# Optimization experiments

Measured on AMD Instinct MI355X. Metric: run time of the kernel, lower is better.

Reference implementation:

```python
import jax, jax.numpy as jnp
import numpy as np

EPS = 1e-8  # torch.cosine_similarity eps


def setup_inputs() -> dict:
    key = jax.random.key(0)
    k1, k2 = jax.random.split(key)
    N, D, TOPIC_E, NT = 4096, 512, 10, 6  # NT = topic_e - topic_s + 1
    x = jax.random.normal(k1, (N, D), dtype=jnp.float32)
    # H mimics the concatenated, abs()'d H_list: (input_feature, topic_e, num_topics)
    H = jax.random.uniform(k2, (D, TOPIC_E, NT), dtype=jnp.float32)
    return {"x": x, "H": H}


def reference(x, H):
    N, D = x.shape
    num_topics = H.shape[2]

    # W_list[n, t, i] = (x @ H[:, :, i])[n, t]
    W_list = jnp.einsum('nd,dti->nti', x, H)          # (N, topic_e, num_topics)
    W_max = jnp.argmax(W_list, axis=1)                # (N, num_topics), int

    # cosine similarity matrix S[a, b] = cos(x[a], x[b]) (symmetric)
    norms = jnp.maximum(jnp.linalg.norm(x, axis=1), EPS)  # (N,)
    xn = x / norms[:, None]
    S = xn @ xn.T                                      # (N, N)

    # topic-match fraction F[a, b] = mean_k [W_max[a,k] == W_max[b,k]] (symmetric)
    comp = (W_max[:, None, :] == W_max[None, :, :])    # (N, N, num_topics) bool
    F = comp.sum(axis=2).astype(jnp.float32) / num_topics

    # C[a, b] = topic_count * sim; new_nodes[b] = mean_a C[a,b] * cat(x[b], x[a])
    C = F * S                                          # (N, N)
    col_mean = C.mean(axis=0)                          # (N,) mean over a
    out_first = x * col_mean[:, None]                  # (N, D): x[b] * mean_a C[a,b]
    out_second = (C.T @ x) / N                         # (N, D): (1/N) sum_a C[a,b] x[a]
    return jnp.concatenate([out_first, out_second], axis=1)  # (N, 2D)
```

## Files before the change

### kernel.cpp

```cpp
#include <hip/hip_runtime.h>
#include <hip/hip_bf16.h>

#define DD 512
#define NTOP 10
#define NTK 6
#define NPAIR 60

typedef float f32x4 __attribute__((ext_vector_type(4)));
typedef short bf16x8 __attribute__((ext_vector_type(8)));
typedef unsigned short us8 __attribute__((ext_vector_type(8)));
typedef unsigned short us4 __attribute__((ext_vector_type(4)));

__device__ __forceinline__ void gload16(const void* g, void* l) {
  __builtin_amdgcn_global_load_lds(
      (const __attribute__((address_space(1))) unsigned int*)g,
      (__attribute__((address_space(3))) unsigned int*)l, 16, 0, 0);
}

__global__ __launch_bounds__(256) void kern_wmax(
    const float* __restrict__ x, const float* __restrict__ H,
    int* __restrict__ codes, float* __restrict__ inv_norm,
    float* __restrict__ col_sum)
{
  __shared__ float xs[4][DD];
  __shared__ float w[4][NPAIR];
  const int wv = threadIdx.x >> 6, lane = threadIdx.x & 63;
  const int n = blockIdx.x * 4 + wv;
  const float* xr = x + (size_t)n * DD;
  float ss = 0.f;
#pragma unroll
  for (int j = 0; j < 2; ++j) {
    float4 v = *(const float4*)(xr + j * 256 + lane * 4);
    *(float4*)&xs[wv][j * 256 + lane * 4] = v;
    ss = fmaf(v.x, v.x, fmaf(v.y, v.y, fmaf(v.z, v.z, fmaf(v.w, v.w, ss))));
  }
#pragma unroll
  for (int off = 32; off; off >>= 1) ss += __shfl_xor(ss, off);
  if (lane == 0) inv_norm[n] = 1.0f / fmaxf(sqrtf(ss), 1e-8f);
  __syncthreads();
  if (lane < NPAIR) {
    float acc = 0.f;
#pragma unroll 8
    for (int d = 0; d < DD; ++d) acc = fmaf(xs[wv][d], H[d * NPAIR + lane], acc);
    w[wv][lane] = acc;
  }
  __syncthreads();
  int myc = 0;
  if (lane < NTK) {
    float best = w[wv][lane];
    int bi = 0;
#pragma unroll
    for (int t = 1; t < NTOP; ++t) {
      float v = w[wv][t * NTK + lane];
      if (v > best) { best = v; bi = t; }
    }
    myc = bi << (4 * lane);
  }
#pragma unroll
  for (int off = 1; off <= 4; off <<= 1) myc |= __shfl_xor(myc, off);
  if (lane == 0) { codes[n] = myc; col_sum[n] = 0.f; }
}

__global__ __launch_bounds__(256) void kern_prep(
    const float* __restrict__ x, const float* __restrict__ inv_norm,
    __hip_bfloat16* __restrict__ xn, __hip_bfloat16* __restrict__ xT, int N)
{
  __shared__ float tile[64][65];
  const int n0 = blockIdx.x * 64, d0 = blockIdx.y * 64;
  const int tid = threadIdx.x;
  const int r = tid >> 2, cseg = (tid & 3) * 16;
  const float* src = x + (size_t)(n0 + r) * DD + d0 + cseg;
  const float invn = inv_norm[n0 + r];
  unsigned short hb[16];
#pragma unroll
  for (int q = 0; q < 4; ++q) {
    float4 v = *(const float4*)(src + q * 4);
    tile[r][cseg + q * 4 + 0] = v.x; tile[r][cseg + q * 4 + 1] = v.y;
    tile[r][cseg + q * 4 + 2] = v.z; tile[r][cseg + q * 4 + 3] = v.w;
    hb[q * 4 + 0] = __builtin_bit_cast(unsigned short, __float2bfloat16(v.x * invn));
    hb[q * 4 + 1] = __builtin_bit_cast(unsigned short, __float2bfloat16(v.y * invn));
    hb[q * 4 + 2] = __builtin_bit_cast(unsigned short, __float2bfloat16(v.z * invn));
    hb[q * 4 + 3] = __builtin_bit_cast(unsigned short, __float2bfloat16(v.w * invn));
  }
  us8 v0, v1;
#pragma unroll
  for (int i = 0; i < 8; ++i) { v0[i] = hb[i]; v1[i] = hb[i + 8]; }
  *(us8*)(xn + (size_t)(n0 + r) * DD + d0 + cseg) = v0;
  *(us8*)(xn + (size_t)(n0 + r) * DD + d0 + cseg + 8) = v1;
  __syncthreads();
  const int drow = tid >> 2, nseg = (tid & 3) * 16;
  unsigned short hb2[16];
#pragma unroll
  for (int i = 0; i < 16; ++i)
    hb2[i] = __builtin_bit_cast(unsigned short, __float2bfloat16(tile[nseg + i][drow]));
  us8 w0, w1;
#pragma unroll
  for (int i = 0; i < 8; ++i) { w0[i] = hb2[i]; w1[i] = hb2[i + 8]; }
  *(us8*)(xT + (size_t)(d0 + drow) * N + n0 + nseg) = w0;
  *(us8*)(xT + (size_t)(d0 + drow) * N + n0 + nseg + 8) = w1;
}

#define GBM 128
#define GBK 64

__global__ __launch_bounds__(512, 4) void kern_gram(
    const __hip_bfloat16* __restrict__ xn, const int* __restrict__ codes,
    __hip_bfloat16* __restrict__ Cb, float* __restrict__ col_sum, int N)
{
  __shared__ __hip_bfloat16 lds[2 * GBM * GBK];
  __shared__ float csA[GBM], csB[GBM];
  __hip_bfloat16* As = lds;
  __hip_bfloat16* Bs = lds + GBM * GBK;
  const int tid = threadIdx.x;

  int idx = blockIdx.x, ai = 0, rem = N / GBM;
  while (idx >= rem) { idx -= rem; ++ai; --rem; }
  const int bi = ai + idx;
  const bool diag = (ai == bi);
  const int a0 = ai * GBM, b0 = bi * GBM;

  if (tid < GBM) { csA[tid] = 0.f; csB[tid] = 0.f; }

  const int lane = tid & 63, wid = tid >> 6;
  const int wr = wid >> 2, wc = wid & 3;

  const f32x4 fz = {0.f, 0.f, 0.f, 0.f};
  f32x4 acc[4][2];
#pragma unroll
  for (int m = 0; m < 4; ++m)
#pragma unroll
    for (int n = 0; n < 2; ++n) acc[m][n] = fz;

  int ldsoff[2]; size_t srcA[2], srcB[2];
#pragma unroll
  for (int i = 0; i < 2; ++i) {
    int p = i * 8192 + tid * 16;
    int row = p >> 7, c = (p >> 4) & 7;
    ldsoff[i] = p;
    size_t cc = (size_t)((c ^ (row & 7)) << 4);
    srcA[i] = (size_t)(a0 + row) * (DD * 2) + cc;
    srcB[i] = (size_t)(b0 + row) * (DD * 2) + cc;
  }
  const char* xc = (const char*)xn;

  for (int kc = 0; kc < DD * 2; kc += GBK * 2) {
#pragma unroll
    for (int i = 0; i < 2; ++i) {
      gload16(xc + srcA[i] + kc, (char*)As + ldsoff[i]);
      gload16(xc + srcB[i] + kc, (char*)Bs + ldsoff[i]);
    }
    __syncthreads();
#pragma unroll
    for (int kk = 0; kk < 2; ++kk) {
      const int kb = kk * 64 + (lane >> 4) * 16;
      bf16x8 af[4], bfr[2];
#pragma unroll
      for (int m = 0; m < 4; ++m) {
        int r = wr * 64 + m * 16 + (lane & 15);
        af[m] = *(const bf16x8*)((const char*)As + r * 128 + (kb ^ ((r & 7) << 4)));
      }
#pragma unroll
      for (int n = 0; n < 2; ++n) {
        int r = wc * 32 + n * 16 + (lane & 15);
        bfr[n] = *(const bf16x8*)((const char*)Bs + r * 128 + (kb ^ ((r & 7) << 4)));
      }
#pragma unroll
      for (int m = 0; m < 4; ++m)
#pragma unroll
        for (int n = 0; n < 2; ++n)
          acc[m][n] = __builtin_amdgcn_mfma_f32_16x16x32_bf16(af[m], bfr[n], acc[m][n], 0, 0, 0);
    }
    __syncthreads();
  }

  char* ldsb = (char*)lds;
  const int rq = (lane >> 4) << 2;
  int cb[2];
#pragma unroll
  for (int n = 0; n < 2; ++n) cb[n] = codes[b0 + wc * 32 + n * 16 + (lane & 15)];

  us4 tvs[4][2];
  float colpart[2] = {0.f, 0.f};
  float rowpart[4][4] = {};
#pragma unroll
  for (int m = 0; m < 4; ++m) {
    int ca[4];
#pragma unroll
    for (int j = 0; j < 4; ++j) ca[j] = codes[a0 + wr * 64 + m * 16 + rq + j];
#pragma unroll
    for (int n = 0; n < 2; ++n) {
      const int col = wc * 32 + n * 16 + (lane & 15);
#pragma unroll
      for (int j = 0; j < 4; ++j) {
        int t = ca[j] ^ cb[n];
        t |= t >> 1; t |= t >> 2;
        t &= 0x111111;
        float f = (float)(6 - __popc(t)) * (1.0f / 6.0f);
        float cv = acc[m][n][j] * f;
        colpart[n] += cv;
        rowpart[m][j] += cv;
        __hip_bfloat16 hv = __float2bfloat16(cv);
        tvs[m][n][j] = __builtin_bit_cast(unsigned short, hv);
        const int row = wr * 64 + m * 16 + rq + j;
        const int boff = row * 256 + ((((col >> 3) ^ (row & 7)) << 4) | ((col & 7) << 1));
        *(__hip_bfloat16*)(ldsb + boff) = hv;
      }
    }
  }
#pragma unroll
  for (int n = 0; n < 2; ++n) {
    float v = colpart[n];
    v += __shfl_xor(v, 16);
    v += __shfl_xor(v, 32);
    if (lane < 16) atomicAdd(&csB[wc * 32 + n * 16 + lane], v);
  }
  if (!diag) {
#pragma unroll
    for (int m = 0; m < 4; ++m)
#pragma unroll
      for (int j = 0; j < 4; ++j) {
        float v = rowpart[m][j];
        v += __shfl_xor(v, 1);
        v += __shfl_xor(v, 2);
        v += __shfl_xor(v, 4);
        v += __shfl_xor(v, 8);
        if ((lane & 15) == 0)
          atomicAdd(&csA[wr * 64 + m * 16 + rq + j], v);
      }
  }
  __syncthreads();
#pragma unroll
  for (int i = 0; i < 4; ++i) {
    const int row = i * 32 + (tid >> 4);
    const int ch = tid & 15;
    us8 v = *(us8*)(ldsb + row * 256 + ((ch ^ (row & 7)) << 4));
    *(us8*)((char*)Cb + ((size_t)(a0 + row) * N + b0) * 2 + (ch << 4)) = v;
  }
  if (!diag) {
    __syncthreads();
#pragma unroll
    for (int m = 0; m < 4; ++m) {
      const int row0 = wr * 64 + m * 16 + rq;
      const int chT = row0 >> 3;
      const int byo = (row0 & 7) << 1;
#pragma unroll
      for (int n = 0; n < 2; ++n) {
        const int col = wc * 32 + n * 16 + (lane & 15);
        *(us4*)(ldsb + col * 256 + (((chT ^ (col & 7)) << 4) | byo)) = tvs[m][n];
      }
    }
    __syncthreads();
#pragma unroll
    for (int i = 0; i < 4; ++i) {
      const int row = i * 32 + (tid >> 4);
      const int ch = tid & 15;
      us8 v = *(us8*)(ldsb + row * 256 + ((ch ^ (row & 7)) << 4));
      *(us8*)((char*)Cb + ((size_t)(b0 + row) * N + a0) * 2 + (ch << 4)) = v;
    }
  }
  if (tid < GBM) {
    atomicAdd(&col_sum[b0 + tid], csB[tid]);
    if (!diag) atomicAdd(&col_sum[a0 + tid], csA[tid]);
  }
}

#define OM 128
#define ON 128
#define OK 64
#define OSK 4
#define ONT 16

__global__ __launch_bounds__(512, 4) void kern_out2(
    const __hip_bfloat16* __restrict__ Cb, const __hip_bfloat16* __restrict__ xT,
    float* __restrict__ part, int N)
{
  __shared__ __hip_bfloat16 As[2][OM * OK];
  __shared__ __hip_bfloat16 Bs[2][ON * OK];
  const int tid = threadIdx.x;
  const int b0 = blockIdx.x * OM;
  const int d0 = blockIdx.y * ON;
  const size_t kbyte0 = (size_t)blockIdx.z * (N / OSK) * 2;
  const int lane = tid & 63, wid = tid >> 6;
  const int wr = wid >> 2, wc = wid & 3;

  const f32x4 fz = {0.f, 0.f, 0.f, 0.f};
  f32x4 acc[4][2];
#pragma unroll
  for (int m = 0; m < 4; ++m)
#pragma unroll
    for (int n = 0; n < 2; ++n) acc[m][n] = fz;

  int ldso[2]; size_t srcA[2], srcB[2];
#pragma unroll
  for (int i = 0; i < 2; ++i) {
    int p = i * 8192 + tid * 16;
    int row = p >> 7, c = (p >> 4) & 7;
    ldso[i] = p;
    size_t cc = (size_t)((c ^ (row & 7)) << 4);
    srcA[i] = (size_t)(b0 + row) * ((size_t)N * 2) + cc + kbyte0;
    srcB[i] = (size_t)(d0 + row) * ((size_t)N * 2) + cc + kbyte0;
  }
  const char* Ac = (const char*)Cb;
  const char* Bc = (const char*)xT;

#define OSTAGE(t, buf) do { \
    const size_t kc = (size_t)(t) * (OK * 2); \
    _Pragma("unroll") \
    for (int i = 0; i < 2; ++i) { \
      gload16(Ac + srcA[i] + kc, (char*)As[buf] + ldso[i]); \
      gload16(Bc + srcB[i] + kc, (char*)Bs[buf] + ldso[i]); \
    } } while (0)

  OSTAGE(0, 0);
  asm volatile("s_waitcnt vmcnt(0)" ::: "memory");
  __builtin_amdgcn_s_barrier();

  for (int t = 0; t < ONT; ++t) {
    const int cur = t & 1;
    if (t + 1 < ONT) OSTAGE(t + 1, cur ^ 1);
    const char* Ab = (const char*)As[cur];
    const char* Bb = (const char*)Bs[cur];
#pragma unroll
    for (int kk = 0; kk < 2; ++kk) {
      const int kb = kk * 64 + (lane >> 4) * 16;
      bf16x8 af[4], bfr[2];
#pragma unroll
      for (int m = 0; m < 4; ++m) {
        int r = wr * 64 + m * 16 + (lane & 15);
        af[m] = *(const bf16x8*)(Ab + r * 128 + (kb ^ ((r & 7) << 4)));
      }
#pragma unroll
      for (int n = 0; n < 2; ++n) {
        int r = wc * 32 + n * 16 + (lane & 15);
        bfr[n] = *(const bf16x8*)(Bb + r * 128 + (kb ^ ((r & 7) << 4)));
      }
#pragma unroll
      for (int m = 0; m < 4; ++m)
#pragma unroll
        for (int n = 0; n < 2; ++n)
          acc[m][n] = __builtin_amdgcn_mfma_f32_16x16x32_bf16(af[m], bfr[n], acc[m][n], 0, 0, 0);
    }
    asm volatile("s_waitcnt vmcnt(0)" ::: "memory");
    __builtin_amdgcn_s_barrier();
  }
#undef OSTAGE

  float* pz = part + (size_t)blockIdx.z * N * DD;
#pragma unroll
  for (int m = 0; m < 4; ++m)
#pragma unroll
    for (int j = 0; j < 4; ++j) {
      int b = b0 + wr * 64 + m * 16 + ((lane >> 4) << 2) + j;
#pragma unroll
      for (int n = 0; n < 2; ++n) {
        int d = d0 + wc * 32 + n * 16 + (lane & 15);
        pz[(size_t)b * DD + d] = acc[m][n][j];
      }
    }
}

__global__ __launch_bounds__(256) void kern_finish(
    const float* __restrict__ x, const float* __restrict__ col_sum,
    const float* __restrict__ part, float* __restrict__ out, int N, int osk)
{
  const int n = blockIdx.x;
  const int tid = threadIdx.x;
  const float invN = 1.0f / (float)N;
  if (tid < 128) {
    const float s = col_sum[n] * invN;
    float4 v = ((const float4*)(x + (size_t)n * DD))[tid];
    v.x *= s; v.y *= s; v.z *= s; v.w *= s;
    ((float4*)(out + (size_t)n * (2 * DD)))[tid] = v;
  } else {
    const int d4 = tid - 128;
    const size_t stride = (size_t)N * DD;
    float4 r = {0.f, 0.f, 0.f, 0.f};
    for (int z = 0; z < osk; ++z) {
      float4 p = *((const float4*)(part + (size_t)z * stride + (size_t)n * DD) + d4);
      r.x += p.x; r.y += p.y; r.z += p.z; r.w += p.w;
    }
    r.x *= invN; r.y *= invN; r.z *= invN; r.w *= invN;
    ((float4*)(out + (size_t)n * (2 * DD) + DD))[d4] = r;
  }
}

extern "C" void kernel_launch(void* const* d_in, const int* in_sizes, int n_in,
                              void* d_out, int out_size, void* d_ws, size_t ws_size,
                              hipStream_t stream) {
  const float* x = (const float*)d_in[0];
  const float* H = (const float*)d_in[1];
  float* out = (float*)d_out;
  const int N = in_sizes[0] / DD;

  char* ws = (char*)d_ws;
  __hip_bfloat16* Cb   = (__hip_bfloat16*)ws;
  __hip_bfloat16* xn16 = (__hip_bfloat16*)(ws + (size_t)N * N * 2);
  __hip_bfloat16* xT16 = xn16 + (size_t)N * DD;
  float* col_sum  = (float*)(xT16 + (size_t)N * DD);
  float* inv_norm = col_sum + N;
  int*   codes    = (int*)(inv_norm + N);
  float* part     = (float*)(codes + N);

  kern_wmax<<<N / 4, 256, 0, stream>>>(x, H, codes, inv_norm, col_sum);
  kern_prep<<<dim3(N / 64, DD / 64), 256, 0, stream>>>(x, inv_norm, xn16, xT16, N);
  const int T = N / GBM;
  kern_gram<<<T * (T + 1) / 2, 512, 0, stream>>>(xn16, codes, Cb, col_sum, N);
  kern_out2<<<dim3(N / OM, DD / ON, OSK), 512, 0, stream>>>(Cb, xT16, part, N);
  kern_finish<<<N, 256, 0, stream>>>(x, col_sum, part, out, N, OSK);
}
```

Measured before the change: 85.71 us.

## Double-buffer LDS tiles in gram kernel to overlap global loads with MFMA

```diff
diff --git a/kernel.cpp b/kernel.cpp
--- a/kernel.cpp
+++ b/kernel.cpp
@@ -102,15 +102,15 @@
 
 #define GBM 128
 #define GBK 64
+#define GNT 8
 
 __global__ __launch_bounds__(512, 4) void kern_gram(
     const __hip_bfloat16* __restrict__ xn, const int* __restrict__ codes,
     __hip_bfloat16* __restrict__ Cb, float* __restrict__ col_sum, int N)
 {
-  __shared__ __hip_bfloat16 lds[2 * GBM * GBK];
+  __shared__ __hip_bfloat16 As[2][GBM * GBK];
+  __shared__ __hip_bfloat16 Bs[2][GBM * GBK];
   __shared__ float csA[GBM], csB[GBM];
-  __hip_bfloat16* As = lds;
-  __hip_bfloat16* Bs = lds + GBM * GBK;
   const int tid = threadIdx.x;
 
   int idx = blockIdx.x, ai = 0, rem = N / GBM;
@@ -143,13 +143,23 @@
   }
   const char* xc = (const char*)xn;
 
-  for (int kc = 0; kc < DD * 2; kc += GBK * 2) {
-#pragma unroll
-    for (int i = 0; i < 2; ++i) {
-      gload16(xc + srcA[i] + kc, (char*)As + ldsoff[i]);
-      gload16(xc + srcB[i] + kc, (char*)Bs + ldsoff[i]);
-    }
-    __syncthreads();
+#define GSTAGE(t, buf) do { \
+    const size_t kc = (size_t)(t) * (GBK * 2); \
+    _Pragma("unroll") \
+    for (int i = 0; i < 2; ++i) { \
+      gload16(xc + srcA[i] + kc, (char*)As[buf] + ldsoff[i]); \
+      gload16(xc + srcB[i] + kc, (char*)Bs[buf] + ldsoff[i]); \
+    } } while (0)
+
+  GSTAGE(0, 0);
+  asm volatile("s_waitcnt vmcnt(0)" ::: "memory");
+  __builtin_amdgcn_s_barrier();
+
+  for (int t = 0; t < GNT; ++t) {
+    const int cur = t & 1;
+    if (t + 1 < GNT) GSTAGE(t + 1, cur ^ 1);
+    const char* Ab = (const char*)As[cur];
+    const char* Bb = (const char*)Bs[cur];
 #pragma unroll
     for (int kk = 0; kk < 2; ++kk) {
       const int kb = kk * 64 + (lane >> 4) * 16;
@@ -157,12 +167,12 @@
 #pragma unroll
       for (int m = 0; m < 4; ++m) {
         int r = wr * 64 + m * 16 + (lane & 15);
-        af[m] = *(const bf16x8*)((const char*)As + r * 128 + (kb ^ ((r & 7) << 4)));
+        af[m] = *(const bf16x8*)(Ab + r * 128 + (kb ^ ((r & 7) << 4)));
       }
 #pragma unroll
       for (int n = 0; n < 2; ++n) {
         int r = wc * 32 + n * 16 + (lane & 15);
-        bfr[n] = *(const bf16x8*)((const char*)Bs + r * 128 + (kb ^ ((r & 7) << 4)));
+        bfr[n] = *(const bf16x8*)(Bb + r * 128 + (kb ^ ((r & 7) << 4)));
       }
 #pragma unroll
       for (int m = 0; m < 4; ++m)
@@ -170,10 +180,12 @@
         for (int n = 0; n < 2; ++n)
           acc[m][n] = __builtin_amdgcn_mfma_f32_16x16x32_bf16(af[m], bfr[n], acc[m][n], 0, 0, 0);
     }
-    __syncthreads();
-  }
-
-  char* ldsb = (char*)lds;
+    asm volatile("s_waitcnt vmcnt(0)" ::: "memory");
+    __builtin_amdgcn_s_barrier();
+  }
+#undef GSTAGE
+
+  char* ldsb = (char*)As;
   const int rq = (lane >> 4) << 2;
   int cb[2];
 #pragma unroll
```

Measured after the change: 92.16 us. 7.5% more time.
